# Performance work log

Hardware: AMD Instinct MI355X
Metric: run time of the kernel (lower is better)

The kernel has to match this reference:

```python
import jax, jax.numpy as jnp
import numpy as np

E = 1024   # embed_dim
H = 16     # num_heads
D = E // H # head_dim = 64
S = 8192   # cache length
LN_EPS = 1e-6  # flax LayerNorm default


def _ln(x, scale, bias):
    m = jnp.mean(x, axis=-1, keepdims=True)
    v = jnp.mean(jnp.square(x - m), axis=-1, keepdims=True)
    return (x - m) * jax.lax.rsqrt(v + LN_EPS) * scale + bias


def setup_inputs() -> dict:
    key = jax.random.key(0)
    ks = jax.random.split(key, 16)
    w = lambda k, shape: jax.random.normal(k, shape, jnp.float32) * 0.02
    return {
        "x": jax.random.normal(ks[0], (E,), jnp.float32),
        "cache": jax.random.normal(ks[1], (2, S, H, D), jnp.float32),
        "Wv": w(ks[2], (E, E)), "bv": jnp.zeros((E,), jnp.float32),
        "Wq": w(ks[3], (E, E)), "bq": jnp.zeros((E,), jnp.float32),
        "Wk": w(ks[4], (E, E)), "bk": jnp.zeros((E,), jnp.float32),
        "Wo": w(ks[5], (E, E)), "bo": jnp.zeros((E,), jnp.float32),
        "W1": w(ks[6], (E, E)), "b1": jnp.zeros((E,), jnp.float32),
        "W2": w(ks[7], (E, E)), "b2": jnp.zeros((E,), jnp.float32),
        "ln1_s": jnp.ones((E,), jnp.float32), "ln1_b": jnp.zeros((E,), jnp.float32),
        "ln2_s": jnp.ones((E,), jnp.float32), "ln2_b": jnp.zeros((E,), jnp.float32),
        "eval_flag": 1,
    }


def reference(x, cache, Wv, bv, Wq, bq, Wk, bk, Wo, bo,
              W1, b1, W2, b2, ln1_s, ln1_b, ln2_s, ln2_b, eval_flag):
    # --- attention with shifting KV cache ---
    v_i = (x @ Wv + bv).reshape(1, H, D)
    q_i = (x @ Wq + bq).reshape(H, D)
    k_i = (x @ Wk + bk).reshape(1, H, D)
    v = jnp.concatenate((cache[0, 1:], v_i), axis=0)  # [S, H, D]
    k = jnp.concatenate((cache[1, 1:], k_i), axis=0)  # [S, H, D]
    mask = jnp.any(v != 0, axis=(1, 2))               # [S]
    attn = jnp.einsum('hd,khd->hk', q_i, k) / jnp.sqrt(jnp.float32(D))
    attn = jnp.where(mask, attn, -jnp.inf)
    attn = jax.nn.softmax(attn, axis=-1)              # [H, S]
    values = jnp.einsum('hk,khd->hd', attn, v).reshape(E)
    out_i = values @ Wo + bo
    new_cache = jnp.stack([v, k])                     # [2, S, H, D]

    # --- residual + LN + FFN (dropout deterministic => identity) ---
    h = _ln(x + out_i, ln1_s, ln1_b)
    ff = jax.nn.relu(h @ W1 + b1) @ W2 + b2
    h = _ln(h + ff, ln2_s, ln2_b)
    return (h, new_cache)
```

## Files before the change

### kernel.cpp

```cpp
#include <hip/hip_runtime.h>
#include <hip/hip_bf16.h>

#define SLEN 8192
#define EDIM 1024
#define NB   512

typedef float f4 __attribute__((ext_vector_type(4)));


__device__ inline float2 blockSum512_2(float2 v, float2* lds) {
#pragma unroll
    for (int off = 32; off; off >>= 1) {
        v.x += __shfl_xor(v.x, off);
        v.y += __shfl_xor(v.y, off);
    }
    int w = threadIdx.x >> 6, ln = threadIdx.x & 63;
    __syncthreads();
    if (ln == 0) lds[w] = v;
    __syncthreads();
    float2 s = {0.f, 0.f};
#pragma unroll
    for (int i = 0; i < 8; ++i) { s.x += lds[i].x; s.y += lds[i].y; }
    return s;
}

__device__ inline float2 blockSum1024_2(float2 v, float2* lds) {
#pragma unroll
    for (int off = 32; off; off >>= 1) {
        v.x += __shfl_xor(v.x, off);
        v.y += __shfl_xor(v.y, off);
    }
    int w = threadIdx.x >> 6, ln = threadIdx.x & 63;
    __syncthreads();
    if (ln == 0) lds[w] = v;
    __syncthreads();
    float2 s = {0.f, 0.f};
#pragma unroll
    for (int i = 0; i < 16; ++i) { s.x += lds[i].x; s.y += lds[i].y; }
    return s;
}

__global__ __launch_bounds__(256) void qkv_partial(
    const float* __restrict__ Wq, const float* __restrict__ Wk,
    const float* __restrict__ Wv, const float* __restrict__ x,
    float* __restrict__ part) {
    int cg_ = blockIdx.x;
    int m = cg_ >> 2;
    const float* W = (m == 0) ? Wq : ((m == 1) ? Wk : Wv);
    int col = (cg_ & 3) * 256 + threadIdx.x;
    int r0 = blockIdx.y * 64;
    float acc = 0.f;
#pragma unroll 16
    for (int r = 0; r < 64; ++r)
        acc = fmaf(x[r0 + r], W[(r0 + r) * EDIM + col], acc);
    part[((size_t)m * 16 + blockIdx.y) * EDIM + col] = acc;
}

__global__ __launch_bounds__(1024) void attn_main(
    const float* __restrict__ cache,
    const float* __restrict__ qkvp,
    const float* __restrict__ bq, const float* __restrict__ bk,
    const float* __restrict__ bv,
    float* __restrict__ nv, float* __restrict__ nk,
    float* __restrict__ l2, float* __restrict__ acc2) {
    __shared__ float qs_l[1024];
    __shared__ float sw[16][16];
    __shared__ float sacc[16][16][64];
    float* kivi = &sacc[0][0][0];

    int tid = threadIdx.x;
    int w = tid >> 6, ld = tid & 63;
    int s = blockIdx.x * 16 + w;

    {
        float v = bq[tid];
#pragma unroll
        for (int sl = 0; sl < 16; ++sl) v += qkvp[sl * EDIM + tid];
        qs_l[tid] = v * 0.125f;
    }
    if (blockIdx.x == NB - 1) {
        float vv_ = bv[tid], kk_ = bk[tid];
#pragma unroll
        for (int sl = 0; sl < 16; ++sl) {
            vv_ += qkvp[(32 + sl) * EDIM + tid];
            kk_ += qkvp[(16 + sl) * EDIM + tid];
        }
        kivi[tid] = vv_;
        kivi[1024 + tid] = kk_;
    }
    __syncthreads();

    bool last = (s >= SLEN - 1);
    f4 vv[4], kv[4], q4[4];
    if (!last) {
        const float* vsrc = cache + (size_t)(s + 1) * EDIM;
        const float* ksrc = cache + (size_t)(SLEN + s + 1) * EDIM;
#pragma unroll
        for (int it = 0; it < 4; ++it)
            vv[it] = *(const f4*)(vsrc + it * 256 + ld * 4);
#pragma unroll
        for (int it = 0; it < 4; ++it)
            kv[it] = *(const f4*)(ksrc + it * 256 + ld * 4);
    } else {
#pragma unroll
        for (int it = 0; it < 4; ++it) {
            vv[it] = *(const f4*)&kivi[it * 256 + ld * 4];
            kv[it] = *(const f4*)&kivi[1024 + it * 256 + ld * 4];
        }
    }
#pragma unroll
    for (int it = 0; it < 4; ++it)
        q4[it] = *(const f4*)&qs_l[it * 256 + ld * 4];

    unsigned nzb = 0u;
#pragma unroll
    for (int it = 0; it < 4; ++it) {
        *(f4*)(nv + (size_t)s * EDIM + it * 256 + ld * 4) = vv[it];
        nzb |= __float_as_uint(vv[it].x) | __float_as_uint(vv[it].y) |
               __float_as_uint(vv[it].z) | __float_as_uint(vv[it].w);
    }
    float sc[4];
#pragma unroll
    for (int it = 0; it < 4; ++it) {
        *(f4*)(nk + (size_t)s * EDIM + it * 256 + ld * 4) = kv[it];
        float d = q4[it].x * kv[it].x + q4[it].y * kv[it].y +
                  q4[it].z * kv[it].z + q4[it].w * kv[it].w;
        d += __shfl_xor(d, 1);
        d += __shfl_xor(d, 2);
        d += __shfl_xor(d, 4);
        d += __shfl_xor(d, 8);
        sc[it] = d;
    }
    if (__ballot(nzb != 0u) == 0ull) {
#pragma unroll
        for (int it = 0; it < 4; ++it) sc[it] = -1e30f;
    }
    float wg[4];
#pragma unroll
    for (int it = 0; it < 4; ++it) wg[it] = __expf(sc[it]);
    if ((ld & 15) == 0) {
#pragma unroll
        for (int it = 0; it < 4; ++it) sw[w][it * 4 + (ld >> 4)] = wg[it];
    }
    __syncthreads();

#pragma unroll
    for (int it = 0; it < 4; ++it) {
        int h = it * 4 + (ld >> 4);
        *(f4*)&sacc[w][h][(ld & 15) * 4] =
            (f4){wg[it] * vv[it].x, wg[it] * vv[it].y, wg[it] * vv[it].z, wg[it] * vv[it].w};
    }
    __syncthreads();

    {
        float a = 0.f;
#pragma unroll
        for (int ww = 0; ww < 16; ++ww) a += sacc[ww][w][ld];
        acc2[(size_t)blockIdx.x * 1024 + w * 64 + ld] = a;
        if (ld == 0) {
            float l = 0.f;
#pragma unroll
            for (int ww = 0; ww < 16; ++ww) l += sw[ww][w];
            l2[blockIdx.x * 16 + w] = l;
        }
    }
}

__global__ __launch_bounds__(256) void attn_red(
    const float* __restrict__ l2, const float* __restrict__ acc2,
    float* __restrict__ l3g, float* __restrict__ acc3) {
    __shared__ float sA[4][64];
    __shared__ float sLl[4][16];
    int cx = blockIdx.x, g = blockIdx.y;
    int t = threadIdx.x, w = t >> 6, ld = t & 63;
    int p0 = g * 64 + w * 16;
    float a = 0.f;
#pragma unroll
    for (int i = 0; i < 16; ++i)
        a += acc2[(size_t)(p0 + i) * 1024 + cx * 64 + ld];
    sA[w][ld] = a;
    if (cx == 0 && ld < 16) {
        float l = 0.f;
#pragma unroll
        for (int i = 0; i < 16; ++i) l += l2[(p0 + i) * 16 + ld];
        sLl[w][ld] = l;
    }
    __syncthreads();
    if (w == 0) {
        acc3[(size_t)g * 1024 + cx * 64 + ld] =
            sA[0][ld] + sA[1][ld] + sA[2][ld] + sA[3][ld];
        if (cx == 0 && ld < 16)
            l3g[g * 16 + ld] = sLl[0][ld] + sLl[1][ld] + sLl[2][ld] + sLl[3][ld];
    }
}

__global__ __launch_bounds__(512) void gemv_wo(
    const float* __restrict__ Wo,
    const float* __restrict__ l3g, const float* __restrict__ acc3,
    float* __restrict__ part) {
    __shared__ float vals[64];
    __shared__ float sred[2][256];
    int by = blockIdx.y;
    int t = threadIdx.x;
    if (t < 64) {
        float a = 0.f, L = 0.f;
#pragma unroll
        for (int g = 0; g < 8; ++g) {
            a += acc3[(size_t)g * 1024 + by * 64 + t];
            L += l3g[g * 16 + by];
        }
        vals[t] = a / L;
    }
    __syncthreads();
    int half = t >> 8, tc = t & 255;
    int col = blockIdx.x * 256 + tc;
    float acc = 0.f;
#pragma unroll 16
    for (int r = 0; r < 32; ++r)
        acc = fmaf(vals[half * 32 + r],
                   Wo[(size_t)(by * 64 + half * 32 + r) * EDIM + col], acc);
    sred[half][tc] = acc;
    __syncthreads();
    if (t < 256)
        part[(size_t)by * EDIM + blockIdx.x * 256 + t] = sred[0][t] + sred[1][t];
}

__global__ __launch_bounds__(512) void gemv_w1(
    const float* __restrict__ W1, const float* __restrict__ gp1,
    const float* __restrict__ bo, const float* __restrict__ x,
    const float* __restrict__ ln1s, const float* __restrict__ ln1b,
    float* __restrict__ h1, float* __restrict__ part) {
    __shared__ float r_l[1024];
    __shared__ float2 red[8];
    __shared__ float vals[64];
    __shared__ float sred[2][256];
    int t = threadIdx.x;
    float2 ss = {0.f, 0.f};
#pragma unroll
    for (int j = 0; j < 2; ++j) {
        int i = t + 512 * j;
        float v = x[i] + bo[i];
#pragma unroll
        for (int sl = 0; sl < 16; ++sl) v += gp1[(size_t)sl * EDIM + i];
        r_l[i] = v;
        ss.x += v; ss.y += v * v;
    }
    float2 s = blockSum512_2(ss, red);
    float mean = s.x * (1.f / 1024.f);
    float var = s.y * (1.f / 1024.f) - mean * mean;
    float rstd = rsqrtf(var + 1e-6f);
    int by = blockIdx.y;
    if (t < 64) {
        int row = by * 64 + t;
        float hv = (r_l[row] - mean) * rstd * ln1s[row] + ln1b[row];
        vals[t] = hv;
        if (blockIdx.x == 0) h1[row] = hv;
    }
    __syncthreads();
    int half = t >> 8, tc = t & 255;
    int col = blockIdx.x * 256 + tc;
    float acc = 0.f;
#pragma unroll 16
    for (int r = 0; r < 32; ++r)
        acc = fmaf(vals[half * 32 + r],
                   W1[(size_t)(by * 64 + half * 32 + r) * EDIM + col], acc);
    sred[half][tc] = acc;
    __syncthreads();
    if (t < 256)
        part[(size_t)by * EDIM + blockIdx.x * 256 + t] = sred[0][t] + sred[1][t];
}

__global__ __launch_bounds__(512) void gemv_w2(
    const float* __restrict__ W2, const float* __restrict__ gp2,
    const float* __restrict__ b1, float* __restrict__ part) {
    __shared__ float vals[64];
    __shared__ float sred[2][256];
    int by = blockIdx.y;
    int t = threadIdx.x;
    if (t < 64) {
        int r = by * 64 + t;
        float v = b1[r];
#pragma unroll
        for (int sl = 0; sl < 16; ++sl) v += gp2[(size_t)sl * EDIM + r];
        vals[t] = fmaxf(v, 0.f);
    }
    __syncthreads();
    int half = t >> 8, tc = t & 255;
    int col = blockIdx.x * 256 + tc;
    float acc = 0.f;
#pragma unroll 16
    for (int r = 0; r < 32; ++r)
        acc = fmaf(vals[half * 32 + r],
                   W2[(size_t)(by * 64 + half * 32 + r) * EDIM + col], acc);
    sred[half][tc] = acc;
    __syncthreads();
    if (t < 256)
        part[(size_t)by * EDIM + blockIdx.x * 256 + t] = sred[0][t] + sred[1][t];
}

__global__ __launch_bounds__(1024) void combine_ln(
    const float* __restrict__ part, const float* __restrict__ bias,
    const float* __restrict__ resid, const float* __restrict__ g,
    const float* __restrict__ b, float* __restrict__ out) {
    __shared__ float2 lds[16];
    int t = threadIdx.x;
    float v = bias[t];
#pragma unroll
    for (int sl = 0; sl < 16; ++sl) v += part[(size_t)sl * EDIM + t];
    float r = resid[t] + v;
    float2 s = blockSum1024_2((float2){r, r * r}, lds);
    float mean = s.x * (1.f / 1024.f);
    float var = s.y * (1.f / 1024.f) - mean * mean;
    out[t] = (r - mean) * rsqrtf(var + 1e-6f) * g[t] + b[t];
}

extern "C" void kernel_launch(void* const* d_in, const int* in_sizes, int n_in,
                              void* d_out, int out_size, void* d_ws, size_t ws_size,
                              hipStream_t stream) {
    const float* x     = (const float*)d_in[0];
    const float* cache = (const float*)d_in[1];
    const float* Wv    = (const float*)d_in[2];
    const float* bv    = (const float*)d_in[3];
    const float* Wq    = (const float*)d_in[4];
    const float* bq    = (const float*)d_in[5];
    const float* Wk    = (const float*)d_in[6];
    const float* bk    = (const float*)d_in[7];
    const float* Wo    = (const float*)d_in[8];
    const float* bo    = (const float*)d_in[9];
    const float* W1    = (const float*)d_in[10];
    const float* b1    = (const float*)d_in[11];
    const float* W2    = (const float*)d_in[12];
    const float* b2    = (const float*)d_in[13];
    const float* ln1s  = (const float*)d_in[14];
    const float* ln1b  = (const float*)d_in[15];
    const float* ln2s  = (const float*)d_in[16];
    const float* ln2b  = (const float*)d_in[17];

    float* out = (float*)d_out;
    float* nv = out + 1024;
    float* nk = out + 1024 + (size_t)SLEN * EDIM;

    float* w    = (float*)d_ws;
    float* qkvp = w;
    float* l2   = qkvp + 48 * 1024;
    float* acc2 = l2 + (size_t)NB * 16;
    float* l3g  = acc2 + (size_t)NB * 1024;
    float* acc3 = l3g + 128;
    float* gp1  = acc3 + 8 * 1024;
    float* h1   = gp1 + 16 * 1024;
    float* gp2  = h1 + 1024;
    float* gp3  = gp2 + 16 * 1024;

    qkv_partial<<<dim3(12, 16), 256, 0, stream>>>(Wq, Wk, Wv, x, qkvp);
    attn_main<<<NB, 1024, 0, stream>>>(cache, qkvp, bq, bk, bv, nv, nk, l2, acc2);
    attn_red<<<dim3(16, 8), 256, 0, stream>>>(l2, acc2, l3g, acc3);
    gemv_wo<<<dim3(4, 16), 512, 0, stream>>>(Wo, l3g, acc3, gp1);
    gemv_w1<<<dim3(4, 16), 512, 0, stream>>>(W1, gp1, bo, x, ln1s, ln1b, h1, gp2);
    gemv_w2<<<dim3(4, 16), 512, 0, stream>>>(W2, gp2, b1, gp3);
    combine_ln<<<1, 1024, 0, stream>>>(gp3, b2, h1, ln2s, ln2b, out);
}
```

Baseline: 50.17 us.

## Process two cache rows per wave in attention and halve block count

Each wave in attn_main now loads and processes two consecutive cache positions, accumulating the exp-weighted values and weight sums in registers before the shared-memory cross-wave reduction. The grid shrinks from 512 to 256 blocks, and the downstream reduction and Wo GEMV are resized to match the fewer partial groups. This is meant to amortise the per-block q setup, barriers and shared-memory reduction over more rows and to shrink the partial-sum traffic. In exchange it uses more registers per thread and leaves fewer blocks to cover memory latency.

```diff
diff --git a/kernel.cpp b/kernel.cpp
--- a/kernel.cpp
+++ b/kernel.cpp
@@ -3,7 +3,7 @@
 
 #define SLEN 8192
 #define EDIM 1024
-#define NB   512
+#define NB   256
 
 typedef float f4 __attribute__((ext_vector_type(4)));
 
@@ -70,7 +70,7 @@
 
     int tid = threadIdx.x;
     int w = tid >> 6, ld = tid & 63;
-    int s = blockIdx.x * 16 + w;
+    int s0 = blockIdx.x * 32 + w * 2;
 
     {
         float v = bq[tid];
@@ -90,65 +90,88 @@
     }
     __syncthreads();
 
-    bool last = (s >= SLEN - 1);
-    f4 vv[4], kv[4], q4[4];
-    if (!last) {
-        const float* vsrc = cache + (size_t)(s + 1) * EDIM;
-        const float* ksrc = cache + (size_t)(SLEN + s + 1) * EDIM;
-#pragma unroll
-        for (int it = 0; it < 4; ++it)
-            vv[it] = *(const f4*)(vsrc + it * 256 + ld * 4);
-#pragma unroll
-        for (int it = 0; it < 4; ++it)
-            kv[it] = *(const f4*)(ksrc + it * 256 + ld * 4);
-    } else {
-#pragma unroll
-        for (int it = 0; it < 4; ++it) {
-            vv[it] = *(const f4*)&kivi[it * 256 + ld * 4];
-            kv[it] = *(const f4*)&kivi[1024 + it * 256 + ld * 4];
+    f4 vv[2][4], kv[2][4], q4[4];
+#pragma unroll
+    for (int p = 0; p < 2; ++p) {
+        int s = s0 + p;
+        if (s < SLEN - 1) {
+            const float* vsrc = cache + (size_t)(s + 1) * EDIM;
+            const float* ksrc = cache + (size_t)(SLEN + s + 1) * EDIM;
+#pragma unroll
+            for (int it = 0; it < 4; ++it)
+                vv[p][it] = *(const f4*)(vsrc + it * 256 + ld * 4);
+#pragma unroll
+            for (int it = 0; it < 4; ++it)
+                kv[p][it] = *(const f4*)(ksrc + it * 256 + ld * 4);
+        } else {
+#pragma unroll
+            for (int it = 0; it < 4; ++it) {
+                vv[p][it] = *(const f4*)&kivi[it * 256 + ld * 4];
+                kv[p][it] = *(const f4*)&kivi[1024 + it * 256 + ld * 4];
+            }
         }
     }
 #pragma unroll
     for (int it = 0; it < 4; ++it)
         q4[it] = *(const f4*)&qs_l[it * 256 + ld * 4];
 
-    unsigned nzb = 0u;
+#pragma unroll
+    for (int p = 0; p < 2; ++p) {
+        int s = s0 + p;
+#pragma unroll
+        for (int it = 0; it < 4; ++it)
+            *(f4*)(nv + (size_t)s * EDIM + it * 256 + ld * 4) = vv[p][it];
+#pragma unroll
+        for (int it = 0; it < 4; ++it)
+            *(f4*)(nk + (size_t)s * EDIM + it * 256 + ld * 4) = kv[p][it];
+    }
+
+    float wgsum[4];
+    f4 acc[4];
 #pragma unroll
     for (int it = 0; it < 4; ++it) {
-        *(f4*)(nv + (size_t)s * EDIM + it * 256 + ld * 4) = vv[it];
-        nzb |= __float_as_uint(vv[it].x) | __float_as_uint(vv[it].y) |
-               __float_as_uint(vv[it].z) | __float_as_uint(vv[it].w);
-    }
-    float sc[4];
-#pragma unroll
-    for (int it = 0; it < 4; ++it) {
-        *(f4*)(nk + (size_t)s * EDIM + it * 256 + ld * 4) = kv[it];
-        float d = q4[it].x * kv[it].x + q4[it].y * kv[it].y +
-                  q4[it].z * kv[it].z + q4[it].w * kv[it].w;
-        d += __shfl_xor(d, 1);
-        d += __shfl_xor(d, 2);
-        d += __shfl_xor(d, 4);
-        d += __shfl_xor(d, 8);
-        sc[it] = d;
-    }
-    if (__ballot(nzb != 0u) == 0ull) {
-#pragma unroll
-        for (int it = 0; it < 4; ++it) sc[it] = -1e30f;
-    }
-    float wg[4];
-#pragma unroll
-    for (int it = 0; it < 4; ++it) wg[it] = __expf(sc[it]);
+        wgsum[it] = 0.f;
+        acc[it] = (f4){0.f, 0.f, 0.f, 0.f};
+    }
+#pragma unroll
+    for (int p = 0; p < 2; ++p) {
+        unsigned nzb = 0u;
+#pragma unroll
+        for (int it = 0; it < 4; ++it)
+            nzb |= __float_as_uint(vv[p][it].x) | __float_as_uint(vv[p][it].y) |
+                   __float_as_uint(vv[p][it].z) | __float_as_uint(vv[p][it].w);
+        float sc[4];
+#pragma unroll
+        for (int it = 0; it < 4; ++it) {
+            float d = q4[it].x * kv[p][it].x + q4[it].y * kv[p][it].y +
+                      q4[it].z * kv[p][it].z + q4[it].w * kv[p][it].w;
+            d += __shfl_xor(d, 1);
+            d += __shfl_xor(d, 2);
+            d += __shfl_xor(d, 4);
+            d += __shfl_xor(d, 8);
+            sc[it] = d;
+        }
+        bool allz = (__ballot(nzb != 0u) == 0ull);
+#pragma unroll
+        for (int it = 0; it < 4; ++it) {
+            float wg = allz ? 0.f : __expf(sc[it]);
+            wgsum[it] += wg;
+            acc[it].x = fmaf(wg, vv[p][it].x, acc[it].x);
+            acc[it].y = fmaf(wg, vv[p][it].y, acc[it].y);
+            acc[it].z = fmaf(wg, vv[p][it].z, acc[it].z);
+            acc[it].w = fmaf(wg, vv[p][it].w, acc[it].w);
+        }
+    }
     if ((ld & 15) == 0) {
 #pragma unroll
-        for (int it = 0; it < 4; ++it) sw[w][it * 4 + (ld >> 4)] = wg[it];
+        for (int it = 0; it < 4; ++it) sw[w][it * 4 + (ld >> 4)] = wgsum[it];
     }
     __syncthreads();
 
 #pragma unroll
     for (int it = 0; it < 4; ++it) {
         int h = it * 4 + (ld >> 4);
-        *(f4*)&sacc[w][h][(ld & 15) * 4] =
-            (f4){wg[it] * vv[it].x, wg[it] * vv[it].y, wg[it] * vv[it].z, wg[it] * vv[it].w};
+        *(f4*)&sacc[w][h][(ld & 15) * 4] = acc[it];
     }
     __syncthreads();
 
@@ -205,7 +228,7 @@
     if (t < 64) {
         float a = 0.f, L = 0.f;
 #pragma unroll
-        for (int g = 0; g < 8; ++g) {
+        for (int g = 0; g < 4; ++g) {
             a += acc3[(size_t)g * 1024 + by * 64 + t];
             L += l3g[g * 16 + by];
         }
@@ -345,15 +368,15 @@
     float* l2   = qkvp + 48 * 1024;
     float* acc2 = l2 + (size_t)NB * 16;
     float* l3g  = acc2 + (size_t)NB * 1024;
-    float* acc3 = l3g + 128;
-    float* gp1  = acc3 + 8 * 1024;
+    float* acc3 = l3g + 64;
+    float* gp1  = acc3 + 4 * 1024;
     float* h1   = gp1 + 16 * 1024;
     float* gp2  = h1 + 1024;
     float* gp3  = gp2 + 16 * 1024;
 
     qkv_partial<<<dim3(12, 16), 256, 0, stream>>>(Wq, Wk, Wv, x, qkvp);
     attn_main<<<NB, 1024, 0, stream>>>(cache, qkvp, bq, bk, bv, nv, nk, l2, acc2);
-    attn_red<<<dim3(16, 8), 256, 0, stream>>>(l2, acc2, l3g, acc3);
+    attn_red<<<dim3(16, 4), 256, 0, stream>>>(l2, acc2, l3g, acc3);
     gemv_wo<<<dim3(4, 16), 512, 0, stream>>>(Wo, l3g, acc3, gp1);
     gemv_w1<<<dim3(4, 16), 512, 0, stream>>>(W1, gp1, bo, x, ln1s, ln1b, h1, gp2);
     gemv_w2<<<dim3(4, 16), 512, 0, stream>>>(W2, gp2, b1, gp3);
```

After: 50.25 us. Within noise of the previous version (+0.2%).
